# Kernel tuning notes

Measured on AMD Instinct MI355X. Metric: run time of the kernel, lower is better.

## Reference

```python
import jax, jax.numpy as jnp
import numpy as np
import math

B, T, D = 8, 1024, 512
WS = 12          # window_size (top-k)
EPS = 1e-5       # BatchNorm eps (eval mode, running stats)
NEG = -1e9


def setup_inputs() -> dict:
    key = jax.random.key(0)
    ks = jax.random.split(key, 13)
    x = jax.random.normal(ks[0], (B, T, D), jnp.float32)
    conv1_w = jax.random.normal(ks[1], (512, 512, 5, 5), jnp.float32) / np.float32(np.sqrt(512 * 25))
    conv1_b = jax.random.normal(ks[2], (512,), jnp.float32) * 0.01
    bn1_g = jax.random.uniform(ks[3], (512,), jnp.float32, 0.5, 1.5)
    bn1_b = jax.random.normal(ks[4], (512,), jnp.float32) * 0.1
    bn1_m = jax.random.normal(ks[5], (512,), jnp.float32) * 0.1
    bn1_v = jax.random.uniform(ks[6], (512,), jnp.float32, 0.5, 1.5)
    conv2_w = jax.random.normal(ks[7], (512, 512, 5, 3), jnp.float32) / np.float32(np.sqrt(512 * 15))
    conv2_b = jax.random.normal(ks[8], (512,), jnp.float32) * 0.01
    bn2_g = jax.random.uniform(ks[9], (512,), jnp.float32, 0.5, 1.5)
    bn2_b = jax.random.normal(ks[10], (512,), jnp.float32) * 0.1
    bn2_m = jax.random.normal(ks[11], (512,), jnp.float32) * 0.1
    bn2_v = jax.random.uniform(ks[12], (512,), jnp.float32, 0.5, 1.5)
    return dict(x=x, conv1_w=conv1_w, conv1_b=conv1_b, bn1_g=bn1_g, bn1_b=bn1_b,
                bn1_m=bn1_m, bn1_v=bn1_v, conv2_w=conv2_w, conv2_b=conv2_b,
                bn2_g=bn2_g, bn2_b=bn2_b, bn2_m=bn2_m, bn2_v=bn2_v)


def _conv_nchw(h, w, b):
    # Conv2d padding=(2,0): pad height by 2 each side, no width padding.
    out = jax.lax.conv_general_dilated(h, w, window_strides=(1, 1),
                                       padding=((2, 2), (0, 0)),
                                       dimension_numbers=('NCHW', 'OIHW', 'NCHW'))
    return out + b[None, :, None, None]


def _bn(h, g, bt, m, v):
    # eval-mode BatchNorm2d with running stats
    inv = jax.lax.rsqrt(v + EPS)
    return (h - m[None, :, None, None]) * (g * inv)[None, :, None, None] + bt[None, :, None, None]


def _pool2(h):
    return jax.lax.reduce_window(h, -jnp.inf, jax.lax.max,
                                 (1, 1, 2, 2), (1, 1, 2, 2), 'VALID')


def reference(x, conv1_w, conv1_b, bn1_g, bn1_b, bn1_m, bn1_v,
              conv2_w, conv2_b, bn2_g, bn2_b, bn2_m, bn2_v):
    b, t, d = x.shape
    # masked local attention scores
    scores = jnp.einsum('btd,bsd->bts', x, x) / math.sqrt(d)  # [B,T,T]
    i = jnp.arange(t)[:, None]
    j = jnp.arange(t)[None, :]
    band = jnp.abs(j - i) <= (WS - 1)  # local band, width 2*WS-1
    scores = jnp.where(band[None], scores, NEG)
    # top-k window select, indices sorted ascending
    _, idx = jax.lax.top_k(scores, WS)           # [B,T,WS]
    ids = jnp.sort(idx, axis=-1)
    # batched gather: out[b,t,k,:] = x[b, ids[b,t,k], :]
    gathered = x[jnp.arange(b)[:, None, None], ids]  # [B,T,WS,D]
    h = gathered.transpose(0, 3, 1, 2)               # [B,512,T,WS]
    # conv encoder
    h = jax.nn.relu(_bn(_conv_nchw(h, conv1_w, conv1_b), bn1_g, bn1_b, bn1_m, bn1_v))
    h = _pool2(h)                                    # [B,512,T/2,4]
    h = jax.nn.relu(_bn(_conv_nchw(h, conv2_w, conv2_b), bn2_g, bn2_b, bn2_m, bn2_v))
    h = _pool2(h)                                    # [B,512,T/4,1]
    return jnp.squeeze(h)                            # [B,512,T/4]
```

## Files before the change

### kernel.cpp

```cpp
#include <hip/hip_runtime.h>
#include <hip/hip_bf16.h>

typedef short bf16x8 __attribute__((ext_vector_type(8)));
typedef float f32x16 __attribute__((ext_vector_type(16)));
typedef unsigned short u16;

__device__ __forceinline__ u16 f2bf(float v) {
    union { __hip_bfloat16 h; u16 u; } cv;
    cv.h = __float2bfloat16(v);
    return cv.u;
}

__device__ __forceinline__ void gld_lds16(const u16* g, u16* l) {
    __builtin_amdgcn_global_load_lds(
        (const __attribute__((address_space(1))) void*)g,
        (__attribute__((address_space(3))) void*)l, 16, 0, 0);
}

__global__ void prep_w1(const float* __restrict__ w, u16* __restrict__ o) {
    int idx = blockIdx.x * 256 + threadIdx.x;
    if (idx >= 25 * 512 * 512) return;
    int e = idx & 7, ocl = (idx >> 3) & 63, c = (idx >> 9) & 3;
    int ocs = (idx >> 11) & 7, T = idx >> 14;
    int icb = T / 25, tap = T - icb * 25;
    int ic = icb * 32 + c * 8 + e;
    int oc = ocs * 64 + ocl;
    int kh = tap / 5, kw = tap - kh * 5;
    o[idx] = f2bf(w[(((size_t)oc * 512 + ic) * 5 + kh) * 5 + kw]);
}

__global__ void prep_w2(const float* __restrict__ w, u16* __restrict__ o) {
    int idx = blockIdx.x * 256 + threadIdx.x;
    if (idx >= 15 * 512 * 512) return;
    int e = idx & 7, ocl = (idx >> 3) & 63, c = (idx >> 9) & 3;
    int ocs = (idx >> 11) & 7, T = idx >> 14;
    int icb = T / 15, tap = T - icb * 15;
    int ic = icb * 32 + c * 8 + e;
    int oc = ocs * 64 + ocl;
    int kh = tap / 3, kw = tap - kh * 3;
    o[idx] = f2bf(w[(((size_t)oc * 512 + ic) * 5 + kh) * 3 + kw]);
}

__global__ void prep_bn(const float* __restrict__ g, const float* __restrict__ b,
                        const float* __restrict__ m, const float* __restrict__ v,
                        float* __restrict__ scale, float* __restrict__ shift) {
    int i = blockIdx.x * 256 + threadIdx.x;
    if (i >= 512) return;
    float s = g[i] * rsqrtf(v[i] + 1e-5f);
    scale[i] = s;
    shift[i] = b[i] - m[i] * s;
}

__global__ void zero_pads(u16* __restrict__ gath, u16* __restrict__ pooled) {
    int idx = blockIdx.x * 256 + threadIdx.x;
    if (idx < 24576) {
        int w = idx % 12, r = idx / 12;
        int h4 = r & 3; r >>= 2;
        int cc = r & 63, b = r >> 6;
        int h = (h4 < 2) ? h4 : 1024 + h4;
        *(int4*)&gath[(((size_t)(b * 64 + cc)) * 12336 + h * 12 + w) * 8] =
            int4{0, 0, 0, 0};
    } else if (idx < 24576 + 8192) {
        int j = idx - 24576;
        int w = j & 3, r = j >> 2;
        int h4 = r & 3; r >>= 2;
        int cc = r & 63, b = r >> 6;
        int hp = (h4 < 2) ? h4 : 512 + h4;
        *(int4*)&pooled[(((size_t)(b * 64 + cc)) * 2064 + hp * 4 + w) * 8] =
            int4{0, 0, 0, 0};
    }
}

__global__ __launch_bounds__(256) void gather_topk(const float* __restrict__ x,
                                                   u16* __restrict__ g) {
    int bt = blockIdx.x;
    int b = bt >> 10, t = bt & 1023;
    const float* xb = x + (size_t)b * 1024 * 512;
    const float* xt = xb + (size_t)t * 512;
    __shared__ float xts[512];
    __shared__ float sc[23];
    __shared__ int sel[12];
    int tid = threadIdx.x;
    for (int i = tid; i < 512; i += 256) xts[i] = xt[i];
    __syncthreads();
    int j0 = t - 11; if (j0 < 0) j0 = 0;
    int j1 = t + 11; if (j1 > 1023) j1 = 1023;
    int C = j1 - j0 + 1;
    int wave = tid >> 6, lane = tid & 63;
    for (int c = wave; c < C; c += 4) {
        const float* xj = xb + (size_t)(j0 + c) * 512;
        double s = 0.0;
        #pragma unroll
        for (int e = 0; e < 8; ++e) {
            int d = lane * 8 + e;
            s += (double)xj[d] * (double)xts[d];
        }
        #pragma unroll
        for (int off = 32; off; off >>= 1) s += __shfl_xor(s, off, 64);
        if (lane == 0) sc[c] = (float)(s / 22.627416997969522);
    }
    __syncthreads();
    if (tid == 0) {
        int cnt = 0;
        for (int c = 0; c < C; ++c) {
            float v = sc[c];
            int r = 0;
            for (int k = 0; k < C; ++k) {
                float u = sc[k];
                r += (u > v) || (u == v && k < c);
            }
            if (r < 12) sel[cnt++] = j0 + c;
        }
    }
    __syncthreads();
    const size_t rowbase = (size_t)(t + 2) * 12;
    for (int i = tid; i < 768; i += 256) {
        int cc = i / 12, s = i - cc * 12;
        const float* src = xb + (size_t)sel[s] * 512 + cc * 8;
        float4 f0 = *(const float4*)src;
        float4 f1 = *(const float4*)(src + 4);
        u16 pk[8] = {f2bf(f0.x), f2bf(f0.y), f2bf(f0.z), f2bf(f0.w),
                     f2bf(f1.x), f2bf(f1.y), f2bf(f1.z), f2bf(f1.w)};
        *(int4*)&g[(((size_t)(b * 64 + cc)) * 12336 + rowbase + s) * 8] =
            *(const int4*)pk;
    }
}


template <int IN_W, int LOG_OW, int KH, int KW, int TH, int HTB, int MF32,
          int ARP, int PLANE, int CPX, bool POOL2E>
__global__ __launch_bounds__(512, 1) void conv_fused(
    const u16* __restrict__ A, const u16* __restrict__ Wt,
    const float* __restrict__ bias, const float* __restrict__ bnsc,
    const float* __restrict__ bnsh, void* __restrict__ outp) {
    constexpr int OW = 1 << LOG_OW;
    constexpr int TAPS = KH * KW;
    constexpr int JC = ARP / 64;
    constexpr int MFR = (32 >> LOG_OW) * IN_W;
    constexpr int SLAB = ARP * 8 + 32;
    __shared__ u16 As_l[2][8 * SLAB];

    const int tid = threadIdx.x;
    const int bid = blockIdx.x;
    const int lb = (bid & 7) * CPX + (bid >> 3);
    const int n0 = (lb & 1) * 256;
    const int mt = lb >> 1;
    const int b = mt / HTB;
    const int h0 = (mt % HTB) * TH;

    const int lane = tid & 63;
    const int wv = tid >> 6;
    const int wm = wv >> 2, wn = wv & 3;
    const int l31 = lane & 31, kgrp = lane >> 5;

    const int pos0 = wm * MF32 * 32 + l31;
    const int rowb0 = (pos0 >> LOG_OW) * IN_W + (pos0 & (OW - 1));
    const int aoffb = kgrp * SLAB + rowb0 * 8;

    const int ocs = (lb & 1) * 4 + wn;
    const u16* wlane = Wt + (size_t)ocs * 2048 + kgrp * 512 + l31 * 8;

    const u16* gAh = A + (((size_t)b * 64) * PLANE + h0 * IN_W + lane) * 8;

    f32x16 acc[MF32][2];
    #pragma unroll
    for (int i = 0; i < MF32; ++i)
        #pragma unroll
        for (int j = 0; j < 2; ++j)
            acc[i][j] = f32x16{0.f,0.f,0.f,0.f,0.f,0.f,0.f,0.f,
                               0.f,0.f,0.f,0.f,0.f,0.f,0.f,0.f};

    #pragma unroll 1
    for (int q = wv; q < 8 * JC; q += 8) {
        int c8 = q / JC, j = q - c8 * JC;
        gld_lds16(gAh + ((size_t)(c8 * PLANE) + j * 64) * 8,
                  &As_l[0][c8 * SLAB + j * 512]);
    }
    bf16x8 wc0 = *(const bf16x8*)(wlane);
    bf16x8 wc1 = *(const bf16x8*)(wlane + 256);
    bf16x8 wc2 = *(const bf16x8*)(wlane + 1024);
    bf16x8 wc3 = *(const bf16x8*)(wlane + 1280);
    bf16x8 wn0 = *(const bf16x8*)(wlane + 16384);
    bf16x8 wn1 = *(const bf16x8*)(wlane + 16384 + 256);
    bf16x8 wn2 = *(const bf16x8*)(wlane + 16384 + 1024);
    bf16x8 wn3 = *(const bf16x8*)(wlane + 16384 + 1280);
    const u16* wpf = wlane + 2 * 16384;
    asm volatile("s_waitcnt vmcnt(0)" ::: "memory");
    __builtin_amdgcn_s_barrier();

    #pragma unroll 1
    for (int cn = 0; cn < 8; ++cn) {
        if (cn < 7) {
            const int chn = cn + 1;
            #pragma unroll 1
            for (int q = wv; q < 8 * JC; q += 8) {
                int c8 = q / JC, j = q - c8 * JC;
                gld_lds16(gAh + ((size_t)((chn * 8 + c8) * PLANE) + j * 64) * 8,
                          &As_l[chn & 1][c8 * SLAB + j * 512]);
            }
        }
        const u16* aBufc = &As_l[cn & 1][0] + aoffb;
        #pragma unroll
        for (int gh = 0; gh < 2; ++gh) {
            const u16* aR = aBufc + gh * 4 * SLAB;
            #pragma unroll
            for (int t = 0; t < TAPS; ++t) {
                bf16x8 wf0 = *(const bf16x8*)(wpf);
                bf16x8 wf1 = *(const bf16x8*)(wpf + 256);
                bf16x8 wf2 = *(const bf16x8*)(wpf + 1024);
                bf16x8 wf3 = *(const bf16x8*)(wpf + 1280);
                wpf += 16384;
                const int kh_ = t / KW;
                const int toff = kh_ * IN_W + (t - kh_ * KW);
                __builtin_amdgcn_s_setprio(1);
                bf16x8 afr[MF32];
                #pragma unroll
                for (int mf = 0; mf < MF32; ++mf)
                    afr[mf] = *(const bf16x8*)(aR + (toff + MFR * mf) * 8);
                #pragma unroll
                for (int mf = 0; mf < MF32; ++mf) {
                    acc[mf][0] = __builtin_amdgcn_mfma_f32_32x32x16_bf16(
                        afr[mf], wc0, acc[mf][0], 0, 0, 0);
                    acc[mf][1] = __builtin_amdgcn_mfma_f32_32x32x16_bf16(
                        afr[mf], wc1, acc[mf][1], 0, 0, 0);
                }
                #pragma unroll
                for (int mf = 0; mf < MF32; ++mf)
                    afr[mf] = *(const bf16x8*)(aR + (toff + MFR * mf) * 8
                                               + 2 * SLAB);
                #pragma unroll
                for (int mf = 0; mf < MF32; ++mf) {
                    acc[mf][0] = __builtin_amdgcn_mfma_f32_32x32x16_bf16(
                        afr[mf], wc2, acc[mf][0], 0, 0, 0);
                    acc[mf][1] = __builtin_amdgcn_mfma_f32_32x32x16_bf16(
                        afr[mf], wc3, acc[mf][1], 0, 0, 0);
                }
                __builtin_amdgcn_s_setprio(0);
                wc0 = wn0; wc1 = wn1; wc2 = wn2; wc3 = wn3;
                wn0 = wf0; wn1 = wf1; wn2 = wf2; wn3 = wf3;
            }
        }
        asm volatile("s_waitcnt vmcnt(8)" ::: "memory");
        __builtin_amdgcn_s_barrier();
    }
    asm volatile("s_waitcnt vmcnt(0)" ::: "memory");

    #pragma unroll
    for (int nf = 0; nf < 2; ++nf) {
        const int oc = n0 + wn * 64 + nf * 32 + l31;
        const float scv = bnsc[oc], shv = bnsh[oc], bi = bias[oc];
        const float shh = fmaf(bi, scv, shv);
        #pragma unroll
        for (int mf = 0; mf < MF32; ++mf) {
            #pragma unroll
            for (int q = 0; q < 4; ++q) {
                if (!POOL2E) {
                    const int r0 = (q & 1) * 2 + (q >> 1) * 8;
                    float mx = fmaxf(
                        fmaxf(acc[mf][nf][r0], acc[mf][nf][r0 + 1]),
                        fmaxf(acc[mf][nf][r0 + 4], acc[mf][nf][r0 + 5]));
                    float v = fmaxf(fmaf(mx, scv, shh), 0.f);
                    const int row0 = (r0 & 3) + 8 * (r0 >> 2) + 4 * kgrp;
                    const int pos = wm * MF32 * 32 + mf * 32 + row0;
                    const int h = h0 + (pos >> LOG_OW);
                    const int w = pos & (OW - 1);
                    const int prow = (2 + (h >> 1)) * 4 + (w >> 1);
                    u16* o = (u16*)outp;
                    o[(((size_t)(b * 64 + (oc >> 3))) * 2064 + prow) * 8 +
                      (oc & 7)] = f2bf(v);
                } else {
                    const int r0 = q * 4;
                    float mx = fmaxf(
                        fmaxf(acc[mf][nf][r0], acc[mf][nf][r0 + 1]),
                        fmaxf(acc[mf][nf][r0 + 2], acc[mf][nf][r0 + 3]));
                    float v = fmaxf(fmaf(mx, scv, shh), 0.f);
                    const int row0 = 8 * (r0 >> 2) + 4 * kgrp;
                    const int pos = wm * 32 + row0;
                    const int pout = (h0 + (pos >> 1)) >> 1;
                    float* o = (float*)outp;
                    o[((size_t)(b * 512 + oc)) * 256 + pout] = v;
                }
            }
        }
    }
}

extern "C" void kernel_launch(void* const* d_in, const int* in_sizes, int n_in,
                              void* d_out, int out_size, void* d_ws, size_t ws_size,
                              hipStream_t stream) {
    const float* x  = (const float*)d_in[0];
    const float* w1 = (const float*)d_in[1];
    const float* b1 = (const float*)d_in[2];
    const float* g1 = (const float*)d_in[3];
    const float* be1 = (const float*)d_in[4];
    const float* m1 = (const float*)d_in[5];
    const float* v1 = (const float*)d_in[6];
    const float* w2 = (const float*)d_in[7];
    const float* b2 = (const float*)d_in[8];
    const float* g2 = (const float*)d_in[9];
    const float* be2 = (const float*)d_in[10];
    const float* m2 = (const float*)d_in[11];
    const float* v2 = (const float*)d_in[12];
    float* out = (float*)d_out;

    char* ws = (char*)d_ws;
    u16* gathered = (u16*)(ws);
    u16* w1t      = (u16*)(ws + 101056512);
    u16* w2t      = (u16*)(ws + 114163712);
    float* bn1s   = (float*)(ws + 122028032);
    float* bn1t   = bn1s + 512;
    float* bn2s   = bn1s + 1024;
    float* bn2t   = bn1s + 1536;
    u16* pooled1  = (u16*)(ws + 122036224);

    prep_w1<<<25600, 256, 0, stream>>>(w1, w1t);
    prep_w2<<<15360, 256, 0, stream>>>(w2, w2t);
    prep_bn<<<2, 256, 0, stream>>>(g1, be1, m1, v1, bn1s, bn1t);
    prep_bn<<<2, 256, 0, stream>>>(g2, be2, m2, v2, bn2s, bn2t);
    zero_pads<<<128, 256, 0, stream>>>(gathered, pooled1);
    gather_topk<<<8192, 256, 0, stream>>>(x, gathered);

    conv_fused<12, 3, 5, 5, 32, 32, 4, 448, 12336, 64, false>
        <<<512, 512, 0, stream>>>(gathered, w1t, b1, bn1s, bn1t, pooled1);
    conv_fused<4, 1, 5, 3, 32, 16, 1, 192, 2064, 32, true>
        <<<256, 512, 0, stream>>>(pooled1, w2t, b2, bn2s, bn2t, out);
}
```

Measured before the change: 889.5 us.

## Software-pipeline conv MFMA loop with ping-pong weights and parallelize top-k selection

The conv kernel's tap loop is restructured so weight fragments are prefetched one tap ahead into even/odd register sets, and A fragments from LDS are loaded one half-step ahead to interleave with the MFMAs. The prefetch depth for weights drops from two taps to one, and the wait before the barrier changes to vmcnt(4). The top-k selection also moves from a single serial thread to a wavefront, where each lane ranks one candidate and a ballot/popcount writes the indices in order. This shortens LDS-to-MFMA stalls and the serial selection cost, at the risk of exposing more global-load latency for weights.

Result: faster. 788.5 us (-11.4%).

```diff
diff --git a/kernel.cpp b/kernel.cpp
--- a/kernel.cpp
+++ b/kernel.cpp
@@ -100,16 +100,24 @@
         if (lane == 0) sc[c] = (float)(s / 22.627416997969522);
     }
     __syncthreads();
-    if (tid == 0) {
-        int cnt = 0;
-        for (int c = 0; c < C; ++c) {
-            float v = sc[c];
+    if (tid < 64) {
+        bool selme = false;
+        float v = (tid < C) ? sc[tid] : 0.f;
+        if (tid < C) {
             int r = 0;
-            for (int k = 0; k < C; ++k) {
-                float u = sc[k];
-                r += (u > v) || (u == v && k < c);
-            }
-            if (r < 12) sel[cnt++] = j0 + c;
+            #pragma unroll
+            for (int k = 0; k < 23; ++k) {
+                if (k < C) {
+                    float u = sc[k];
+                    r += (u > v) || (u == v && k < tid);
+                }
+            }
+            selme = (r < 12);
+        }
+        unsigned long long m = __ballot(selme);
+        if (selme) {
+            int posn = __popcll(m & ((1ull << tid) - 1ull));
+            sel[posn] = j0 + tid;
         }
     }
     __syncthreads();
@@ -138,6 +146,7 @@
     constexpr int JC = ARP / 64;
     constexpr int MFR = (32 >> LOG_OW) * IN_W;
     constexpr int SLAB = ARP * 8 + 32;
+    constexpr int NB = 2 * TAPS;
     __shared__ u16 As_l[2][8 * SLAB];
 
     const int tid = threadIdx.x;
@@ -176,15 +185,11 @@
         gld_lds16(gAh + ((size_t)(c8 * PLANE) + j * 64) * 8,
                   &As_l[0][c8 * SLAB + j * 512]);
     }
-    bf16x8 wc0 = *(const bf16x8*)(wlane);
-    bf16x8 wc1 = *(const bf16x8*)(wlane + 256);
-    bf16x8 wc2 = *(const bf16x8*)(wlane + 1024);
-    bf16x8 wc3 = *(const bf16x8*)(wlane + 1280);
-    bf16x8 wn0 = *(const bf16x8*)(wlane + 16384);
-    bf16x8 wn1 = *(const bf16x8*)(wlane + 16384 + 256);
-    bf16x8 wn2 = *(const bf16x8*)(wlane + 16384 + 1024);
-    bf16x8 wn3 = *(const bf16x8*)(wlane + 16384 + 1280);
-    const u16* wpf = wlane + 2 * 16384;
+    bf16x8 wE0 = *(const bf16x8*)(wlane);
+    bf16x8 wE1 = *(const bf16x8*)(wlane + 256);
+    bf16x8 wE2 = *(const bf16x8*)(wlane + 1024);
+    bf16x8 wE3 = *(const bf16x8*)(wlane + 1280);
+    bf16x8 wO0, wO1, wO2, wO3;
     asm volatile("s_waitcnt vmcnt(0)" ::: "memory");
     __builtin_amdgcn_s_barrier();
 
@@ -200,47 +205,62 @@
             }
         }
         const u16* aBufc = &As_l[cn & 1][0] + aoffb;
-        #pragma unroll
-        for (int gh = 0; gh < 2; ++gh) {
+        const u16* wch = wlane + ((size_t)cn * NB + 1) * 16384;
+        bf16x8 afA[MF32], afB[MF32];
+        #pragma unroll
+        for (int mf = 0; mf < MF32; ++mf)
+            afA[mf] = *(const bf16x8*)(aBufc + MFR * mf * 8);
+        #pragma unroll
+        for (int bi = 0; bi < NB; ++bi) {
+            const int gh = bi / TAPS, t = bi - gh * TAPS;
+            const int kh_ = t / KW;
+            const int toff = kh_ * IN_W + (t - kh_ * KW);
             const u16* aR = aBufc + gh * 4 * SLAB;
-            #pragma unroll
-            for (int t = 0; t < TAPS; ++t) {
-                bf16x8 wf0 = *(const bf16x8*)(wpf);
-                bf16x8 wf1 = *(const bf16x8*)(wpf + 256);
-                bf16x8 wf2 = *(const bf16x8*)(wpf + 1024);
-                bf16x8 wf3 = *(const bf16x8*)(wpf + 1280);
-                wpf += 16384;
-                const int kh_ = t / KW;
-                const int toff = kh_ * IN_W + (t - kh_ * KW);
-                __builtin_amdgcn_s_setprio(1);
-                bf16x8 afr[MF32];
+            const u16* wS = wch + (size_t)bi * 16384;
+            if (bi & 1) {
+                wE0 = *(const bf16x8*)(wS);
+                wE1 = *(const bf16x8*)(wS + 256);
+                wE2 = *(const bf16x8*)(wS + 1024);
+                wE3 = *(const bf16x8*)(wS + 1280);
+            } else {
+                wO0 = *(const bf16x8*)(wS);
+                wO1 = *(const bf16x8*)(wS + 256);
+                wO2 = *(const bf16x8*)(wS + 1024);
+                wO3 = *(const bf16x8*)(wS + 1280);
+            }
+            #pragma unroll
+            for (int mf = 0; mf < MF32; ++mf)
+                afB[mf] = *(const bf16x8*)(aR + (toff + MFR * mf) * 8 + 2 * SLAB);
+            __builtin_amdgcn_s_setprio(1);
+            #pragma unroll
+            for (int mf = 0; mf < MF32; ++mf) {
+                acc[mf][0] = __builtin_amdgcn_mfma_f32_32x32x16_bf16(
+                    afA[mf], (bi & 1) ? wO0 : wE0, acc[mf][0], 0, 0, 0);
+                acc[mf][1] = __builtin_amdgcn_mfma_f32_32x32x16_bf16(
+                    afA[mf], (bi & 1) ? wO1 : wE1, acc[mf][1], 0, 0, 0);
+            }
+            __builtin_amdgcn_s_setprio(0);
+            if (bi + 1 < NB) {
+                const int bn2 = bi + 1;
+                const int ghn = bn2 / TAPS, tn = bn2 - ghn * TAPS;
+                const int khn = tn / KW;
+                const int toffn = khn * IN_W + (tn - khn * KW);
+                const u16* aRn = aBufc + ghn * 4 * SLAB;
                 #pragma unroll
                 for (int mf = 0; mf < MF32; ++mf)
-                    afr[mf] = *(const bf16x8*)(aR + (toff + MFR * mf) * 8);
-                #pragma unroll
-                for (int mf = 0; mf < MF32; ++mf) {
-                    acc[mf][0] = __builtin_amdgcn_mfma_f32_32x32x16_bf16(
-                        afr[mf], wc0, acc[mf][0], 0, 0, 0);
-                    acc[mf][1] = __builtin_amdgcn_mfma_f32_32x32x16_bf16(
-                        afr[mf], wc1, acc[mf][1], 0, 0, 0);
-                }
-                #pragma unroll
-                for (int mf = 0; mf < MF32; ++mf)
-                    afr[mf] = *(const bf16x8*)(aR + (toff + MFR * mf) * 8
-                                               + 2 * SLAB);
-                #pragma unroll
-                for (int mf = 0; mf < MF32; ++mf) {
-                    acc[mf][0] = __builtin_amdgcn_mfma_f32_32x32x16_bf16(
-                        afr[mf], wc2, acc[mf][0], 0, 0, 0);
-                    acc[mf][1] = __builtin_amdgcn_mfma_f32_32x32x16_bf16(
-                        afr[mf], wc3, acc[mf][1], 0, 0, 0);
-                }
-                __builtin_amdgcn_s_setprio(0);
-                wc0 = wn0; wc1 = wn1; wc2 = wn2; wc3 = wn3;
-                wn0 = wf0; wn1 = wf1; wn2 = wf2; wn3 = wf3;
-            }
-        }
-        asm volatile("s_waitcnt vmcnt(8)" ::: "memory");
+                    afA[mf] = *(const bf16x8*)(aRn + (toffn + MFR * mf) * 8);
+            }
+            __builtin_amdgcn_s_setprio(1);
+            #pragma unroll
+            for (int mf = 0; mf < MF32; ++mf) {
+                acc[mf][0] = __builtin_amdgcn_mfma_f32_32x32x16_bf16(
+                    afB[mf], (bi & 1) ? wO2 : wE2, acc[mf][0], 0, 0, 0);
+                acc[mf][1] = __builtin_amdgcn_mfma_f32_32x32x16_bf16(
+                    afB[mf], (bi & 1) ? wO3 : wE3, acc[mf][1], 0, 0, 0);
+            }
+            __builtin_amdgcn_s_setprio(0);
+        }
+        asm volatile("s_waitcnt vmcnt(4)" ::: "memory");
         __builtin_amdgcn_s_barrier();
     }
     asm volatile("s_waitcnt vmcnt(0)" ::: "memory");
@@ -248,8 +268,8 @@
     #pragma unroll
     for (int nf = 0; nf < 2; ++nf) {
         const int oc = n0 + wn * 64 + nf * 32 + l31;
-        const float scv = bnsc[oc], shv = bnsh[oc], bi = bias[oc];
-        const float shh = fmaf(bi, scv, shv);
+        const float scv = bnsc[oc], shv = bnsh[oc], bi2 = bias[oc];
+        const float shh = fmaf(bi2, scv, shv);
         #pragma unroll
         for (int mf = 0; mf < MF32; ++mf) {
             #pragma unroll
```
